# Kernel tuning notes

Measured on AMD Instinct MI355X. Metric: run time of the kernel, lower is better.

The kernel has to match this reference:

```python
import jax, jax.numpy as jnp
import numpy as np

B, T, HID = 1, 2048, 4096
H, KVH, D = 32, 8, 128
N_REP = H // KVH
SCALE = D ** -0.5
EPS = 1e-6
THETA = 10000.0
TOPK, SINK, WIN = 256, 16, 256


def _rms_norm(x, w):
    var = jnp.mean(x * x, axis=-1, keepdims=True)
    return w * (x * jax.lax.rsqrt(var + EPS))


def _rotate_half(x):
    x1, x2 = x[..., : D // 2], x[..., D // 2 :]
    return jnp.concatenate([-x2, x1], axis=-1)


def setup_inputs() -> dict:
    key = jax.random.key(0)
    ks = jax.random.split(key, 6)
    hidden_states = jax.random.normal(ks[0], (B, T, HID), jnp.float32)
    Wq = jax.random.normal(ks[1], (HID, H * D), jnp.float32) * 0.02
    Wkv = jax.random.normal(ks[2], (HID, KVH * D), jnp.float32) * 0.02
    Wo = jax.random.normal(ks[3], (H * D, HID), jnp.float32) * 0.02
    q_norm_w = jnp.ones((D,), jnp.float32)
    k_norm_w = jnp.ones((D,), jnp.float32)
    # standard RoPE tables, theta=10000
    inv_freq = 1.0 / (THETA ** (jnp.arange(0, D, 2, dtype=jnp.float32) / D))
    freqs = jnp.arange(T, dtype=jnp.float32)[:, None] * inv_freq[None, :]  # (T, D/2)
    emb = jnp.concatenate([freqs, freqs], axis=-1)  # (T, D)
    cos = jnp.cos(emb)[None]  # (1, T, D)
    sin = jnp.sin(emb)[None]
    return {"hidden_states": hidden_states, "Wq": Wq, "Wkv": Wkv, "Wo": Wo,
            "q_norm_w": q_norm_w, "k_norm_w": k_norm_w, "cos": cos, "sin": sin}


def reference(hidden_states, Wq, Wkv, Wo, q_norm_w, k_norm_w, cos, sin):
    b, t, _ = hidden_states.shape
    s = t
    # projections -> (b, h, t, d)
    q = (hidden_states @ Wq).reshape(b, t, H, D).transpose(0, 2, 1, 3)
    kv = (hidden_states @ Wkv).reshape(b, t, KVH, D).transpose(0, 2, 1, 3)
    # qk RMSNorm per head_dim
    q = _rms_norm(q, q_norm_w)
    k = _rms_norm(kv, k_norm_w)
    v = kv  # latent KV: value shares the latent projection (no norm / rope)
    # rotary, cos/sin unsqueezed at head dim
    c = cos[:, None]  # (1,1,T,D)
    sn = sin[:, None]
    q = q * c + _rotate_half(q) * sn
    k = k * c + _rotate_half(k) * sn
    # GQA expansion
    k = jnp.repeat(k, N_REP, axis=1)
    v = jnp.repeat(v, N_REP, axis=1)
    # dense scores (reference path)
    scores = jnp.einsum("bhtd,bhsd->bhts", q, k) * SCALE  # (b,h,t,s)
    # ---- sparse DSA mask: sink | local window | per-query top-k, then causal ----
    q_idx = jnp.arange(t)
    k_idx = jnp.arange(s)
    sink = (k_idx < SINK)[None, None, None, :]
    local = (jnp.abs(q_idx[:, None] - k_idx[None, :]) <= WIN)[None, None]
    kth = jax.lax.top_k(scores, TOPK)[0][..., -1:]  # k-th largest per query
    topk_keep = scores >= kth
    causal_ok = (k_idx[None, :] <= q_idx[:, None])[None, None]
    keep = (sink | local | topk_keep) & causal_ok
    scores = jnp.where(keep, scores, -jnp.inf)
    attn = jax.nn.softmax(scores, axis=-1)
    out = jnp.einsum("bhts,bhsd->bhtd", attn, v)
    out = out.transpose(0, 2, 1, 3).reshape(b, t, H * D)
    return out @ Wo
```

## Files before the change

kernel.cpp:

```cpp
#include <hip/hip_runtime.h>
#include <hip/hip_bf16.h>

#define H 32
#define KVH 8
#define D 128
#define T 2048
#define HID 4096
#define TOPK 256
#define SINK 16
#define WIN 256
#define SCALE 0.08838834764831845f
#define NPROJ 5120

#define SWZ(row, b) ((b) ^ (((row) & 7) << 4))

#define AS3(p) ((__attribute__((address_space(3))) void*)(p))
#define AS1(p) ((const __attribute__((address_space(1))) void*)(p))

typedef __attribute__((ext_vector_type(4))) float f32x4;
typedef __attribute__((ext_vector_type(8))) short short8;

__device__ __forceinline__ unsigned short f2bf(float f) {
  unsigned int b = __float_as_uint(f);
  b += 0x7FFFu + ((b >> 16) & 1u);
  return (unsigned short)(b >> 16);
}
__device__ __forceinline__ float bf2f(unsigned short u) {
  return __uint_as_float(((unsigned int)u) << 16);
}
__device__ __forceinline__ float ldf(const void* p, long i, bool b16) {
  return b16 ? bf2f(((const unsigned short*)p)[i]) : ((const float*)p)[i];
}
__device__ __forceinline__ bool bf16_mode(const unsigned int* probe) {
  return *probe == 0x3F803F80u;
}

__global__ void cvt_kernel(const void* __restrict__ src, unsigned short* __restrict__ dst,
                           long n, const unsigned int* probe) {
  bool b16 = bf16_mode(probe);
  long stride = (long)gridDim.x * blockDim.x;
  for (long i = (long)blockIdx.x * blockDim.x + threadIdx.x; i * 8 < n; i += stride) {
    long o = i * 8;
    if (b16) {
      *(uint4*)(dst + o) = *(const uint4*)((const unsigned short*)src + o);
    } else {
      const float* s = (const float*)src + o;
      float4 f0 = *(const float4*)s;
      float4 f1 = *(const float4*)(s + 4);
      uint4 v;
      v.x = (unsigned int)f2bf(f0.x) | ((unsigned int)f2bf(f0.y) << 16);
      v.y = (unsigned int)f2bf(f0.z) | ((unsigned int)f2bf(f0.w) << 16);
      v.z = (unsigned int)f2bf(f1.x) | ((unsigned int)f2bf(f1.y) << 16);
      v.w = (unsigned int)f2bf(f1.z) | ((unsigned int)f2bf(f1.w) << 16);
      *(uint4*)(dst + o) = v;
    }
  }
}

__global__ __launch_bounds__(256) void cvt_t(const void* __restrict__ src,
    unsigned short* __restrict__ dst, int R, int Cc, const unsigned int* probe) {
  __shared__ float tile[64][65];
  bool b16 = bf16_mode(probe);
  int r0 = blockIdx.y * 64, c0 = blockIdx.x * 64;
  int tid = threadIdx.x;
  int tr = tid >> 3;
  int tc8 = (tid & 7) * 8;
#pragma unroll
  for (int p = 0; p < 2; ++p) {
    int row = tr + p * 32;
    if (b16) {
      const unsigned short* s = (const unsigned short*)src + (size_t)(r0 + row) * Cc + c0 + tc8;
      uint4 d = *(const uint4*)s;
      const unsigned short* dv = (const unsigned short*)&d;
#pragma unroll
      for (int j = 0; j < 8; ++j) tile[row][tc8 + j] = bf2f(dv[j]);
    } else {
      const float* s = (const float*)src + (size_t)(r0 + row) * Cc + c0 + tc8;
      float4 f0 = *(const float4*)s;
      float4 f1 = *(const float4*)(s + 4);
      tile[row][tc8 + 0] = f0.x; tile[row][tc8 + 1] = f0.y;
      tile[row][tc8 + 2] = f0.z; tile[row][tc8 + 3] = f0.w;
      tile[row][tc8 + 4] = f1.x; tile[row][tc8 + 5] = f1.y;
      tile[row][tc8 + 6] = f1.z; tile[row][tc8 + 7] = f1.w;
    }
  }
  __syncthreads();
#pragma unroll
  for (int p = 0; p < 2; ++p) {
    int oc = tr + p * 32;
    unsigned short tmp[8];
#pragma unroll
    for (int j = 0; j < 8; ++j) tmp[j] = f2bf(tile[tc8 + j][oc]);
    *(uint4*)(dst + (size_t)(c0 + oc) * R + r0 + tc8) = *(uint4*)tmp;
  }
}

__global__ __launch_bounds__(256) void gemm_bf16(
    const unsigned short* __restrict__ A, const unsigned short* __restrict__ Bt,
    void* __restrict__ C, int M, int N, int K, const unsigned int* probe, int outmode) {
  __shared__ alignas(16) unsigned short As[128 * 32];
  __shared__ alignas(16) unsigned short Bs[128 * 32];
  int n0 = blockIdx.x * 128, m0 = blockIdx.y * 128;
  int tid = threadIdx.x;
  int w = tid >> 6, l = tid & 63;
  int wm = (w >> 1) * 64, wn = (w & 1) * 64;
  int lr = l & 15, lg = l >> 4;

  int srow0 = (w * 2 + 0) * 16 + (l >> 2);
  int srow1 = (w * 2 + 1) * 16 + (l >> 2);
  int cch = l & 3;
  int sf0 = (srow0 ^ (srow0 >> 2)) & 3;
  int sf1 = (srow1 ^ (srow1 >> 2)) & 3;
  const unsigned short* gA0 = A + (size_t)(m0 + srow0) * K + ((cch ^ sf0) * 8);
  const unsigned short* gA1 = A + (size_t)(m0 + srow1) * K + ((cch ^ sf1) * 8);
  const unsigned short* gB0 = Bt + (size_t)(n0 + srow0) * K + ((cch ^ sf0) * 8);
  const unsigned short* gB1 = Bt + (size_t)(n0 + srow1) * K + ((cch ^ sf1) * 8);
  unsigned short* lA0 = As + (w * 2 + 0) * 16 * 32;
  unsigned short* lA1 = As + (w * 2 + 1) * 16 * 32;
  unsigned short* lB0 = Bs + (w * 2 + 0) * 16 * 32;
  unsigned short* lB1 = Bs + (w * 2 + 1) * 16 * 32;

  const unsigned short* pa[4];
  const unsigned short* pb[4];
#pragma unroll
  for (int i = 0; i < 4; ++i) {
    int ra = wm + i * 16 + lr;
    int fa = (ra ^ (ra >> 2)) & 3;
    pa[i] = As + ra * 32 + ((lg ^ fa) * 8);
    int rb = wn + i * 16 + lr;
    int fb = (rb ^ (rb >> 2)) & 3;
    pb[i] = Bs + rb * 32 + ((lg ^ fb) * 8);
  }

  f32x4 zero = {0.f, 0.f, 0.f, 0.f};
  f32x4 acc[4][4];
#pragma unroll
  for (int i = 0; i < 4; ++i)
#pragma unroll
    for (int j = 0; j < 4; ++j) acc[i][j] = zero;

  for (int k0 = 0; k0 < K; k0 += 32) {
    __builtin_amdgcn_global_load_lds(AS1(gA0 + k0), AS3(lA0), 16, 0, 0);
    __builtin_amdgcn_global_load_lds(AS1(gA1 + k0), AS3(lA1), 16, 0, 0);
    __builtin_amdgcn_global_load_lds(AS1(gB0 + k0), AS3(lB0), 16, 0, 0);
    __builtin_amdgcn_global_load_lds(AS1(gB1 + k0), AS3(lB1), 16, 0, 0);
    __syncthreads();
    short8 a[4], b[4];
#pragma unroll
    for (int i = 0; i < 4; ++i) {
      a[i] = *(const short8*)pa[i];
      b[i] = *(const short8*)pb[i];
    }
#pragma unroll
    for (int i = 0; i < 4; ++i)
#pragma unroll
      for (int j = 0; j < 4; ++j)
        acc[i][j] = __builtin_amdgcn_mfma_f32_16x16x32_bf16(a[i], b[j], acc[i][j], 0, 0, 0);
    __syncthreads();
  }
  bool b16out = (outmode == 1) || (outmode == 2 && bf16_mode(probe));
#pragma unroll
  for (int i = 0; i < 4; ++i)
#pragma unroll
    for (int j = 0; j < 4; ++j)
#pragma unroll
      for (int r = 0; r < 4; ++r) {
        int row = m0 + wm + i * 16 + lg * 4 + r;
        int col = n0 + wn + j * 16 + lr;
        float v = acc[i][j][r];
        if (b16out) ((unsigned short*)C)[(size_t)row * N + col] = f2bf(v);
        else ((float*)C)[(size_t)row * N + col] = v;
      }
}

__global__ __launch_bounds__(256) void qk_prep(
    const unsigned short* __restrict__ Proj, const void* nw, const void* cosp, const void* sinp,
    unsigned short* __restrict__ Qh, const unsigned int* probe) {
  bool b16 = bf16_mode(probe);
  int w = threadIdx.x >> 6, l = threadIdx.x & 63;
  int gw = blockIdx.x * 4 + w;
  int t = gw >> 5, h = gw & 31;
  const unsigned short* x = Proj + (size_t)t * NPROJ + h * D;
  float x1 = bf2f(x[l]), x2 = bf2f(x[l + 64]);
  float s = x1 * x1 + x2 * x2;
  for (int m = 32; m; m >>= 1) s += __shfl_xor(s, m);
  float inv = rsqrtf(s * (1.0f / D) + 1e-6f);
  float w1 = ldf(nw, l, b16), w2 = ldf(nw, l + 64, b16);
  float c1 = ldf(cosp, (long)t * D + l, b16), c2 = ldf(cosp, (long)t * D + l + 64, b16);
  float s1 = ldf(sinp, (long)t * D + l, b16), s2 = ldf(sinp, (long)t * D + l + 64, b16);
  float xn1 = x1 * inv * w1, xn2 = x2 * inv * w2;
  unsigned short* o = Qh + (size_t)h * T * D + (size_t)t * D;
  o[l] = f2bf(SCALE * (xn1 * c1 - xn2 * s1));
  o[l + 64] = f2bf(SCALE * (xn2 * c2 + xn1 * s2));
}

__global__ __launch_bounds__(256) void kv_prep(
    const unsigned short* __restrict__ Proj, const void* nw, const void* cosp, const void* sinp,
    unsigned short* __restrict__ Kh, unsigned short* __restrict__ Vt, const unsigned int* probe) {
  bool b16 = bf16_mode(probe);
  int w = threadIdx.x >> 6, l = threadIdx.x & 63;
  int gw = blockIdx.x * 4 + w;
  int t = gw >> 3, h = gw & 7;
  const unsigned short* x = Proj + (size_t)t * NPROJ + (H * D) + h * D;
  float x1 = bf2f(x[l]), x2 = bf2f(x[l + 64]);
  Vt[(size_t)h * D * T + (size_t)l * T + t] = x[l];
  Vt[(size_t)h * D * T + (size_t)(l + 64) * T + t] = x[l + 64];
  float s = x1 * x1 + x2 * x2;
  for (int m = 32; m; m >>= 1) s += __shfl_xor(s, m);
  float inv = rsqrtf(s * (1.0f / D) + 1e-6f);
  float w1 = ldf(nw, l, b16), w2 = ldf(nw, l + 64, b16);
  float c1 = ldf(cosp, (long)t * D + l, b16), c2 = ldf(cosp, (long)t * D + l + 64, b16);
  float s1 = ldf(sinp, (long)t * D + l, b16), s2 = ldf(sinp, (long)t * D + l + 64, b16);
  float xn1 = x1 * inv * w1, xn2 = x2 * inv * w2;
  unsigned short* o = Kh + (size_t)h * T * D + (size_t)t * D;
  o[l] = f2bf(xn1 * c1 - xn2 * s1);
  o[l + 64] = f2bf(xn2 * c2 + xn1 * s2);
}

__global__ __launch_bounds__(1024, 8) void attn_kernel(
    const unsigned short* __restrict__ Qh, const unsigned short* __restrict__ Kh,
    const unsigned short* __restrict__ Vt, unsigned short* __restrict__ attn_out) {
  __shared__ alignas(16) unsigned short sc[16][2048];
  __shared__ alignas(16) unsigned short qt[16 * 128];
  __shared__ alignas(16) float part[8][64][4];
  __shared__ float zinv[16];
  int t0 = blockIdx.x * 16;
  int h = blockIdx.y;
  int hk = h >> 2;
  int tid = threadIdx.x;
  int w = tid >> 6, l = tid & 63;
  int lr = l & 15, lg = l >> 4;
  f32x4 zero = {0.f, 0.f, 0.f, 0.f};
  char* scB = (char*)sc;

  {
    int row = tid >> 6;
    int bir = (tid & 63) * 4;
    const unsigned int* qsrc = (const unsigned int*)(Qh + (size_t)h * (T * D) + (size_t)t0 * D);
    *(unsigned int*)((char*)qt + row * 256 + SWZ(row, bir)) = qsrc[tid];
  }
  __syncthreads();

  short8 aq[4];
#pragma unroll
  for (int kk = 0; kk < 4; ++kk)
    aq[kk] = *(const short8*)((const char*)qt + lr * 256 + SWZ(lr, kk * 64 + lg * 16));
  const unsigned short* Kbase = Kh + (size_t)hk * (T * D);
  for (int st = w; st < 128; st += 16) {
    f32x4 acc = zero;
#pragma unroll
    for (int kk = 0; kk < 4; ++kk) {
      short8 kf = *(const short8*)(Kbase + (size_t)(st * 16 + lr) * D + kk * 32 + lg * 8);
      acc = __builtin_amdgcn_mfma_f32_16x16x32_bf16(kf, aq[kk], acc, 0, 0, 0);
    }
    uint2 pk;
    pk.x = (unsigned int)f2bf(acc[0]) | ((unsigned int)f2bf(acc[1]) << 16);
    pk.y = (unsigned int)f2bf(acc[2]) | ((unsigned int)f2bf(acc[3]) << 16);
    *(uint2*)(scB + lr * 4096 + SWZ(lr, st * 32 + lg * 8)) = pk;
  }
  __syncthreads();

  {
    int row = w, tq = t0 + row;
    int rsw = (row & 7) << 4;
    char* rb = scB + row * 4096;
    unsigned int klo[16], khi[16];
#pragma unroll
    for (int i = 0; i < 16; ++i) {
      unsigned int b = *(const unsigned int*)(rb + ((256 * i + 4 * l) ^ rsw));
      unsigned int m = (b >> 15) & 0x00010001u;
      unsigned int kk = b ^ (0x80008000u | (m * 0x7FFFu));
      klo[i] = kk & 0xFFFFu;
      khi[i] = kk >> 16;
    }
    unsigned int lo = 0, hi = 0xFFFFu;
    while (lo < hi) {
      unsigned int mid = (lo + hi + 1u) >> 1;
      int c = 0;
#pragma unroll
      for (int i = 0; i < 16; ++i) {
        c += __popcll(__ballot(klo[i] >= mid));
        c += __popcll(__ballot(khi[i] >= mid));
      }
      if (c >= TOPK) lo = mid; else hi = mid - 1;
    }
    unsigned int thr = lo;
    unsigned int mA = 0, mB = 0, kmax = 0;
#pragma unroll
    for (int i = 0; i < 16; ++i) {
      int s0 = 128 * i + 2 * l;
      bool kp0 = (s0 <= tq) && (s0 < SINK || s0 + WIN >= tq || klo[i] >= thr);
      bool kp1 = (s0 + 1 <= tq) && (s0 + 1 < SINK || s0 + 1 + WIN >= tq || khi[i] >= thr);
      if (kp0) { mA |= (1u << i); kmax = kmax > klo[i] ? kmax : klo[i]; }
      if (kp1) { mB |= (1u << i); kmax = kmax > khi[i] ? kmax : khi[i]; }
    }
    for (int m = 32; m; m >>= 1) {
      unsigned int o = (unsigned int)__shfl_xor((int)kmax, m);
      kmax = kmax > o ? kmax : o;
    }
    unsigned int mb = (kmax & 0x8000u) ? (kmax ^ 0x8000u) : ((~kmax) & 0xFFFFu);
    float mx = bf2f((unsigned short)mb);
    float z = 0.f;
    int lim = (t0 + 15) >> 7;
#pragma unroll
    for (int i = 0; i < 16; ++i) if (i <= lim) {
      unsigned int k0 = klo[i], k1 = khi[i];
      unsigned int b0 = (k0 & 0x8000u) ? (k0 ^ 0x8000u) : ((~k0) & 0xFFFFu);
      unsigned int b1 = (k1 & 0x8000u) ? (k1 ^ 0x8000u) : ((~k1) & 0xFFFFu);
      float e0 = ((mA >> i) & 1u) ? __expf(bf2f((unsigned short)b0) - mx) : 0.f;
      float e1 = ((mB >> i) & 1u) ? __expf(bf2f((unsigned short)b1) - mx) : 0.f;
      z += e0 + e1;
      unsigned int pw = (unsigned int)f2bf(e0) | ((unsigned int)f2bf(e1) << 16);
      *(unsigned int*)(rb + ((256 * i + 4 * l) ^ rsw)) = pw;
    }
    for (int m = 32; m; m >>= 1) z += __shfl_xor(z, m);
    if (l == 0) zinv[row] = 1.0f / z;
  }
  __syncthreads();

  {
    int half = w >> 3;
    int d0 = (w & 7) * 16;
    const unsigned short* Vbase = Vt + (size_t)hk * (D * T);
    const char* prb = scB + lr * 4096;
    int psw = (lr & 7) << 4;
    f32x4 o0 = zero, o1 = zero;
    int ks_end = (t0 + 47) >> 5;
    int ks_endE = (ks_end + 1) & ~1;
    int kmid = ((ks_endE >> 1) + 1) & ~1;
    int ksA = half ? kmid : 0;
    int ksB = half ? ks_endE : kmid;
    for (int ks = ksA; ks < ksB; ks += 2) {
      short8 pa0 = *(const short8*)(prb + ((ks * 64 + lg * 16) ^ psw));
      short8 pa1 = *(const short8*)(prb + (((ks + 1) * 64 + lg * 16) ^ psw));
      short8 vb0 = *(const short8*)(Vbase + (size_t)(d0 + lr) * T + ks * 32 + lg * 8);
      short8 vb1 = *(const short8*)(Vbase + (size_t)(d0 + lr) * T + (ks + 1) * 32 + lg * 8);
      o0 = __builtin_amdgcn_mfma_f32_16x16x32_bf16(vb0, pa0, o0, 0, 0, 0);
      o1 = __builtin_amdgcn_mfma_f32_16x16x32_bf16(vb1, pa1, o1, 0, 0, 0);
    }
    f32x4 oo;
#pragma unroll
    for (int r = 0; r < 4; ++r) oo[r] = o0[r] + o1[r];
    if (half) *(f32x4*)(&part[w & 7][l][0]) = oo;
    __syncthreads();
    if (!half) {
      f32x4 po = *(const f32x4*)(&part[w & 7][l][0]);
      float rz = zinv[lr];
      unsigned short tmp[4];
#pragma unroll
      for (int r = 0; r < 4; ++r) tmp[r] = f2bf((oo[r] + po[r]) * rz);
      unsigned short* dst = attn_out + (size_t)(t0 + lr) * (H * D) + h * D + d0 + lg * 4;
      *(uint2*)dst = *(uint2*)tmp;
    }
  }
}

extern "C" void kernel_launch(void* const* d_in, const int* in_sizes, int n_in,
                              void* d_out, int out_size, void* d_ws, size_t ws_size,
                              hipStream_t stream) {
  (void)in_sizes; (void)n_in; (void)out_size; (void)ws_size;
  const void* hs = d_in[0];
  const void* Wq = d_in[1];
  const void* Wkv = d_in[2];
  const void* Wo = d_in[3];
  const unsigned int* probe = (const unsigned int*)d_in[4];
  const void* knw = d_in[5];
  const void* cosp = d_in[6];
  const void* sinp = d_in[7];

  char* ws = (char*)d_ws;
  unsigned short* WqT_bf = (unsigned short*)(ws);
  unsigned short* WkvT_bf= (unsigned short*)(ws + 33554432);
  unsigned short* WoT_bf = (unsigned short*)(ws + 41943040);
  unsigned short* hid_bf = (unsigned short*)(ws + 75497472);
  unsigned short* Proj_bf= (unsigned short*)(ws + 92274688);
  unsigned short* Qh     = (unsigned short*)(ws + 134217728);
  unsigned short* Kh     = (unsigned short*)(ws + 150994944);
  unsigned short* Vt     = (unsigned short*)(ws + 155189248);
  unsigned short* attn_bf= (unsigned short*)(ws + 159383552);

  hipLaunchKernelGGL(cvt_kernel, dim3(1024), dim3(256), 0, stream, hs, hid_bf, (long)T * HID, probe);
  hipLaunchKernelGGL(cvt_t, dim3(64, 64), dim3(256), 0, stream, Wq, WqT_bf, HID, H * D, probe);
  hipLaunchKernelGGL(cvt_t, dim3(16, 64), dim3(256), 0, stream, Wkv, WkvT_bf, HID, KVH * D, probe);
  hipLaunchKernelGGL(cvt_t, dim3(64, 64), dim3(256), 0, stream, Wo, WoT_bf, H * D, HID, probe);

  hipLaunchKernelGGL(gemm_bf16, dim3(40, 16), dim3(256), 0, stream,
                     hid_bf, WqT_bf, (void*)Proj_bf, 2048, NPROJ, 4096,
                     (const unsigned int*)nullptr, 1);

  hipLaunchKernelGGL(qk_prep, dim3(16384), dim3(256), 0, stream, Proj_bf, d_in[4], cosp, sinp, Qh, probe);
  hipLaunchKernelGGL(kv_prep, dim3(4096), dim3(256), 0, stream, Proj_bf, knw, cosp, sinp, Kh, Vt, probe);

  hipLaunchKernelGGL(attn_kernel, dim3(128, 32), dim3(1024), 0, stream, Qh, Kh, Vt, attn_bf);

  hipLaunchKernelGGL(gemm_bf16, dim3(32, 16), dim3(256), 0, stream,
                     attn_bf, WoT_bf, d_out, 2048, 4096, 4096, probe, 2);
}
```

Before: 764.3 us.

## Swizzle GEMM block order, narrow top-k bisection range, unroll attention loops

```diff
diff --git a/kernel.cpp b/kernel.cpp
--- a/kernel.cpp
+++ b/kernel.cpp
@@ -100,7 +100,11 @@
     void* __restrict__ C, int M, int N, int K, const unsigned int* probe, int outmode) {
   __shared__ alignas(16) unsigned short As[128 * 32];
   __shared__ alignas(16) unsigned short Bs[128 * 32];
-  int n0 = blockIdx.x * 128, m0 = blockIdx.y * 128;
+  int lin = blockIdx.x;
+  int qq = (int)gridDim.x >> 3;
+  int swz = (lin & 7) * qq + (lin >> 3);
+  int nx = N >> 7;
+  int n0 = (swz % nx) * 128, m0 = (swz / nx) * 128;
   int tid = threadIdx.x;
   int w = tid >> 6, l = tid & 63;
   int wm = (w >> 1) * 64, wn = (w & 1) * 64;
@@ -217,6 +221,9 @@
   o[l + 64] = f2bf(xn2 * c2 + xn1 * s2);
 }
 
+#define K16(X) X(0) X(1) X(2) X(3) X(4) X(5) X(6) X(7) \
+               X(8) X(9) X(10) X(11) X(12) X(13) X(14) X(15)
+
 __global__ __launch_bounds__(1024, 8) void attn_kernel(
     const unsigned short* __restrict__ Qh, const unsigned short* __restrict__ Kh,
     const unsigned short* __restrict__ Vt, unsigned short* __restrict__ attn_out) {
@@ -241,78 +248,104 @@
   }
   __syncthreads();
 
-  short8 aq[4];
-#pragma unroll
-  for (int kk = 0; kk < 4; ++kk)
-    aq[kk] = *(const short8*)((const char*)qt + lr * 256 + SWZ(lr, kk * 64 + lg * 16));
-  const unsigned short* Kbase = Kh + (size_t)hk * (T * D);
-  for (int st = w; st < 128; st += 16) {
-    f32x4 acc = zero;
-#pragma unroll
-    for (int kk = 0; kk < 4; ++kk) {
-      short8 kf = *(const short8*)(Kbase + (size_t)(st * 16 + lr) * D + kk * 32 + lg * 8);
-      acc = __builtin_amdgcn_mfma_f32_16x16x32_bf16(kf, aq[kk], acc, 0, 0, 0);
-    }
-    uint2 pk;
-    pk.x = (unsigned int)f2bf(acc[0]) | ((unsigned int)f2bf(acc[1]) << 16);
-    pk.y = (unsigned int)f2bf(acc[2]) | ((unsigned int)f2bf(acc[3]) << 16);
-    *(uint2*)(scB + lr * 4096 + SWZ(lr, st * 32 + lg * 8)) = pk;
+  {
+    short8 aq[4];
+#pragma unroll
+    for (int kk = 0; kk < 4; ++kk)
+      aq[kk] = *(const short8*)((const char*)qt + lr * 256 + SWZ(lr, kk * 64 + lg * 16));
+    const unsigned short* Kbase = Kh + (size_t)hk * (T * D);
+#pragma unroll 2
+    for (int st = w; st < 128; st += 16) {
+      f32x4 acc = zero;
+#pragma unroll
+      for (int kk = 0; kk < 4; ++kk) {
+        short8 kf = *(const short8*)(Kbase + (size_t)(st * 16 + lr) * D + kk * 32 + lg * 8);
+        acc = __builtin_amdgcn_mfma_f32_16x16x32_bf16(kf, aq[kk], acc, 0, 0, 0);
+      }
+      uint2 pk;
+      pk.x = (unsigned int)f2bf(acc[0]) | ((unsigned int)f2bf(acc[1]) << 16);
+      pk.y = (unsigned int)f2bf(acc[2]) | ((unsigned int)f2bf(acc[3]) << 16);
+      *(uint2*)(scB + lr * 4096 + SWZ(lr, st * 32 + lg * 8)) = pk;
+    }
   }
   __syncthreads();
 
   {
     int row = w, tq = t0 + row;
     int rsw = (row & 7) << 4;
+    int lim = (t0 + 15) >> 7;
     char* rb = scB + row * 4096;
-    unsigned int klo[16], khi[16];
-#pragma unroll
-    for (int i = 0; i < 16; ++i) {
-      unsigned int b = *(const unsigned int*)(rb + ((256 * i + 4 * l) ^ rsw));
-      unsigned int m = (b >> 15) & 0x00010001u;
-      unsigned int kk = b ^ (0x80008000u | (m * 0x7FFFu));
-      klo[i] = kk & 0xFFFFu;
-      khi[i] = kk >> 16;
-    }
-    unsigned int lo = 0, hi = 0xFFFFu;
+
+#define DECLK(i) unsigned int klo##i, khi##i;
+    K16(DECLK)
+#undef DECLK
+
+#define LOADK(i) { \
+      unsigned int b = *(const unsigned int*)(rb + ((256 * (i) + 4 * l) ^ rsw)); \
+      unsigned int m = (b >> 15) & 0x00010001u; \
+      b ^= (0x80008000u | (m * 0x7FFFu)); \
+      klo##i = b & 0xFFFFu; khi##i = b >> 16; }
+    K16(LOADK)
+#undef LOADK
+
+    unsigned int um = 0;
+#define MAXK(i) { um = um > klo##i ? um : klo##i; um = um > khi##i ? um : khi##i; }
+    K16(MAXK)
+#undef MAXK
+    for (int m = 32; m; m >>= 1) {
+      unsigned int o = (unsigned int)__shfl_xor((int)um, m);
+      um = um > o ? um : o;
+    }
+
+    unsigned int mid, lo, hi;
+    int cnt;
+#define CNT1(i) cnt += (int)__popcll(__ballot(klo##i >= mid)) + \
+                       (int)__popcll(__ballot(khi##i >= mid));
+    unsigned int probe = um > 2048u ? um - 2048u : 0u;
+    mid = probe; cnt = 0;
+    K16(CNT1)
+    if (cnt >= TOPK) { lo = probe; hi = um; }
+    else { lo = 0u; hi = probe - 1u; }
     while (lo < hi) {
-      unsigned int mid = (lo + hi + 1u) >> 1;
-      int c = 0;
-#pragma unroll
-      for (int i = 0; i < 16; ++i) {
-        c += __popcll(__ballot(klo[i] >= mid));
-        c += __popcll(__ballot(khi[i] >= mid));
-      }
-      if (c >= TOPK) lo = mid; else hi = mid - 1;
-    }
+      mid = (lo + hi + 1u) >> 1;
+      cnt = 0;
+      K16(CNT1)
+      if (cnt >= TOPK) lo = mid; else hi = mid - 1u;
+    }
+#undef CNT1
     unsigned int thr = lo;
-    unsigned int mA = 0, mB = 0, kmax = 0;
-#pragma unroll
-    for (int i = 0; i < 16; ++i) {
-      int s0 = 128 * i + 2 * l;
-      bool kp0 = (s0 <= tq) && (s0 < SINK || s0 + WIN >= tq || klo[i] >= thr);
-      bool kp1 = (s0 + 1 <= tq) && (s0 + 1 < SINK || s0 + 1 + WIN >= tq || khi[i] >= thr);
-      if (kp0) { mA |= (1u << i); kmax = kmax > klo[i] ? kmax : klo[i]; }
-      if (kp1) { mB |= (1u << i); kmax = kmax > khi[i] ? kmax : khi[i]; }
-    }
+
+    int ca0 = (tq - 2 * l) >> 7;
+    int ca1 = (tq - 2 * l - 1) >> 7;
+    int wa0 = (tq - WIN - 2 * l + 127) >> 7;
+    int wa1 = (tq - WIN - 2 * l - 1 + 127) >> 7;
+    bool snk = (l < 8);
+    unsigned int mA = 0, mB = 0, mk = 0;
+#define MASKK(i) if ((i) <= lim) { \
+      bool k0 = ((i) <= ca0) && ((((i) == 0) && snk) || ((i) >= wa0) || (klo##i >= thr)); \
+      bool k1 = ((i) <= ca1) && ((((i) == 0) && snk) || ((i) >= wa1) || (khi##i >= thr)); \
+      if (k0) { mA |= (1u << (i)); mk = mk > klo##i ? mk : klo##i; } \
+      if (k1) { mB |= (1u << (i)); mk = mk > khi##i ? mk : khi##i; } }
+    K16(MASKK)
+#undef MASKK
     for (int m = 32; m; m >>= 1) {
-      unsigned int o = (unsigned int)__shfl_xor((int)kmax, m);
-      kmax = kmax > o ? kmax : o;
-    }
-    unsigned int mb = (kmax & 0x8000u) ? (kmax ^ 0x8000u) : ((~kmax) & 0xFFFFu);
+      unsigned int o = (unsigned int)__shfl_xor((int)mk, m);
+      mk = mk > o ? mk : o;
+    }
+    unsigned int mb = (mk & 0x8000u) ? (mk ^ 0x8000u) : ((~mk) & 0xFFFFu);
     float mx = bf2f((unsigned short)mb);
+
     float z = 0.f;
-    int lim = (t0 + 15) >> 7;
-#pragma unroll
-    for (int i = 0; i < 16; ++i) if (i <= lim) {
-      unsigned int k0 = klo[i], k1 = khi[i];
-      unsigned int b0 = (k0 & 0x8000u) ? (k0 ^ 0x8000u) : ((~k0) & 0xFFFFu);
-      unsigned int b1 = (k1 & 0x8000u) ? (k1 ^ 0x8000u) : ((~k1) & 0xFFFFu);
-      float e0 = ((mA >> i) & 1u) ? __expf(bf2f((unsigned short)b0) - mx) : 0.f;
-      float e1 = ((mB >> i) & 1u) ? __expf(bf2f((unsigned short)b1) - mx) : 0.f;
-      z += e0 + e1;
-      unsigned int pw = (unsigned int)f2bf(e0) | ((unsigned int)f2bf(e1) << 16);
-      *(unsigned int*)(rb + ((256 * i + 4 * l) ^ rsw)) = pw;
-    }
+#define EXPK(i) if ((i) <= lim) { \
+      unsigned int b0 = (klo##i & 0x8000u) ? (klo##i ^ 0x8000u) : ((~klo##i) & 0xFFFFu); \
+      unsigned int b1 = (khi##i & 0x8000u) ? (khi##i ^ 0x8000u) : ((~khi##i) & 0xFFFFu); \
+      float e0 = ((mA >> (i)) & 1u) ? __expf(bf2f((unsigned short)b0) - mx) : 0.f; \
+      float e1 = ((mB >> (i)) & 1u) ? __expf(bf2f((unsigned short)b1) - mx) : 0.f; \
+      z += e0 + e1; \
+      *(unsigned int*)(rb + ((256 * (i) + 4 * l) ^ rsw)) = \
+          (unsigned int)f2bf(e0) | ((unsigned int)f2bf(e1) << 16); }
+    K16(EXPK)
+#undef EXPK
     for (int m = 32; m; m >>= 1) z += __shfl_xor(z, m);
     if (l == 0) zinv[row] = 1.0f / z;
   }
@@ -330,6 +363,7 @@
     int kmid = ((ks_endE >> 1) + 1) & ~1;
     int ksA = half ? kmid : 0;
     int ksB = half ? ks_endE : kmid;
+#pragma unroll 2
     for (int ks = ksA; ks < ksB; ks += 2) {
       short8 pa0 = *(const short8*)(prb + ((ks * 64 + lg * 16) ^ psw));
       short8 pa1 = *(const short8*)(prb + (((ks + 1) * 64 + lg * 16) ^ psw));
@@ -384,7 +418,7 @@
   hipLaunchKernelGGL(cvt_t, dim3(16, 64), dim3(256), 0, stream, Wkv, WkvT_bf, HID, KVH * D, probe);
   hipLaunchKernelGGL(cvt_t, dim3(64, 64), dim3(256), 0, stream, Wo, WoT_bf, H * D, HID, probe);
 
-  hipLaunchKernelGGL(gemm_bf16, dim3(40, 16), dim3(256), 0, stream,
+  hipLaunchKernelGGL(gemm_bf16, dim3(640), dim3(256), 0, stream,
                      hid_bf, WqT_bf, (void*)Proj_bf, 2048, NPROJ, 4096,
                      (const unsigned int*)nullptr, 1);
 
@@ -393,6 +427,6 @@
 
   hipLaunchKernelGGL(attn_kernel, dim3(128, 32), dim3(1024), 0, stream, Qh, Kh, Vt, attn_bf);
 
-  hipLaunchKernelGGL(gemm_bf16, dim3(32, 16), dim3(256), 0, stream,
+  hipLaunchKernelGGL(gemm_bf16, dim3(512), dim3(256), 0, stream,
                      attn_bf, WoT_bf, d_out, 2048, 4096, 4096, probe, 2);
 }
```

Measured after the change: 786.3 us. 2.9% more time.

## Swizzle GEMM blocks across XCDs, fold log2e into Q, and narrow the top-k search

Applied to the files above, without the earlier changes.

```diff
diff --git a/kernel.cpp b/kernel.cpp
--- a/kernel.cpp
+++ b/kernel.cpp
@@ -9,7 +9,7 @@
 #define TOPK 256
 #define SINK 16
 #define WIN 256
-#define SCALE 0.08838834764831845f
+#define SCALE2 0.12753102600893415f
 #define NPROJ 5120
 
 #define SWZ(row, b) ((b) ^ (((row) & 7) << 4))
@@ -100,7 +100,11 @@
     void* __restrict__ C, int M, int N, int K, const unsigned int* probe, int outmode) {
   __shared__ alignas(16) unsigned short As[128 * 32];
   __shared__ alignas(16) unsigned short Bs[128 * 32];
-  int n0 = blockIdx.x * 128, m0 = blockIdx.y * 128;
+  int lin = blockIdx.x;
+  int qq = (int)gridDim.x >> 3;
+  int swz = (lin & 7) * qq + (lin >> 3);
+  int nx = N >> 7;
+  int n0 = (swz % nx) * 128, m0 = (swz / nx) * 128;
   int tid = threadIdx.x;
   int w = tid >> 6, l = tid & 63;
   int wm = (w >> 1) * 64, wn = (w & 1) * 64;
@@ -190,8 +194,8 @@
   float s1 = ldf(sinp, (long)t * D + l, b16), s2 = ldf(sinp, (long)t * D + l + 64, b16);
   float xn1 = x1 * inv * w1, xn2 = x2 * inv * w2;
   unsigned short* o = Qh + (size_t)h * T * D + (size_t)t * D;
-  o[l] = f2bf(SCALE * (xn1 * c1 - xn2 * s1));
-  o[l + 64] = f2bf(SCALE * (xn2 * c2 + xn1 * s2));
+  o[l] = f2bf(SCALE2 * (xn1 * c1 - xn2 * s1));
+  o[l + 64] = f2bf(SCALE2 * (xn2 * c2 + xn1 * s2));
 }
 
 __global__ __launch_bounds__(256) void kv_prep(
@@ -241,77 +245,120 @@
   }
   __syncthreads();
 
-  short8 aq[4];
-#pragma unroll
-  for (int kk = 0; kk < 4; ++kk)
-    aq[kk] = *(const short8*)((const char*)qt + lr * 256 + SWZ(lr, kk * 64 + lg * 16));
-  const unsigned short* Kbase = Kh + (size_t)hk * (T * D);
-  for (int st = w; st < 128; st += 16) {
-    f32x4 acc = zero;
-#pragma unroll
-    for (int kk = 0; kk < 4; ++kk) {
-      short8 kf = *(const short8*)(Kbase + (size_t)(st * 16 + lr) * D + kk * 32 + lg * 8);
-      acc = __builtin_amdgcn_mfma_f32_16x16x32_bf16(kf, aq[kk], acc, 0, 0, 0);
-    }
-    uint2 pk;
-    pk.x = (unsigned int)f2bf(acc[0]) | ((unsigned int)f2bf(acc[1]) << 16);
-    pk.y = (unsigned int)f2bf(acc[2]) | ((unsigned int)f2bf(acc[3]) << 16);
-    *(uint2*)(scB + lr * 4096 + SWZ(lr, st * 32 + lg * 8)) = pk;
+  {
+    short8 aq[4];
+#pragma unroll
+    for (int kk = 0; kk < 4; ++kk)
+      aq[kk] = *(const short8*)((const char*)qt + lr * 256 + SWZ(lr, kk * 64 + lg * 16));
+    const unsigned short* Kbase = Kh + (size_t)hk * (T * D);
+#pragma unroll 2
+    for (int st = w; st < 128; st += 16) {
+      const unsigned short* kp = Kbase + (size_t)(st * 16 + lr) * D + lg * 8;
+      short8 kf0 = *(const short8*)(kp);
+      short8 kf1 = *(const short8*)(kp + 32);
+      short8 kf2 = *(const short8*)(kp + 64);
+      short8 kf3 = *(const short8*)(kp + 96);
+      f32x4 accA = zero, accB = zero;
+      accA = __builtin_amdgcn_mfma_f32_16x16x32_bf16(kf0, aq[0], accA, 0, 0, 0);
+      accB = __builtin_amdgcn_mfma_f32_16x16x32_bf16(kf1, aq[1], accB, 0, 0, 0);
+      accA = __builtin_amdgcn_mfma_f32_16x16x32_bf16(kf2, aq[2], accA, 0, 0, 0);
+      accB = __builtin_amdgcn_mfma_f32_16x16x32_bf16(kf3, aq[3], accB, 0, 0, 0);
+      uint2 pk;
+      pk.x = (unsigned int)f2bf(accA[0] + accB[0]) | ((unsigned int)f2bf(accA[1] + accB[1]) << 16);
+      pk.y = (unsigned int)f2bf(accA[2] + accB[2]) | ((unsigned int)f2bf(accA[3] + accB[3]) << 16);
+      *(uint2*)(scB + lr * 4096 + SWZ(lr, st * 32 + lg * 8)) = pk;
+    }
   }
   __syncthreads();
 
   {
     int row = w, tq = t0 + row;
     int rsw = (row & 7) << 4;
+    int lim = (t0 + 15) >> 7;
     char* rb = scB + row * 4096;
     unsigned int klo[16], khi[16];
 #pragma unroll
     for (int i = 0; i < 16; ++i) {
       unsigned int b = *(const unsigned int*)(rb + ((256 * i + 4 * l) ^ rsw));
       unsigned int m = (b >> 15) & 0x00010001u;
-      unsigned int kk = b ^ (0x80008000u | (m * 0x7FFFu));
-      klo[i] = kk & 0xFFFFu;
-      khi[i] = kk >> 16;
-    }
-    unsigned int lo = 0, hi = 0xFFFFu;
+      unsigned int kk2 = b ^ (0x80008000u | (m * 0x7FFFu));
+      klo[i] = kk2 & 0xFFFFu;
+      khi[i] = kk2 >> 16;
+    }
+    unsigned int um = 0;
+#pragma unroll
+    for (int i = 0; i < 16; ++i) {
+      unsigned int a_ = klo[i] > khi[i] ? klo[i] : khi[i];
+      um = um > a_ ? um : a_;
+    }
+    for (int m = 32; m; m >>= 1) {
+      unsigned int o = (unsigned int)__shfl_xor((int)um, m);
+      um = um > o ? um : o;
+    }
+    unsigned int lo = 0, hi = um;
+    {
+      unsigned int mid = um > 192u ? um - 192u : 1u;
+      int cnt = 0;
+#pragma unroll
+      for (int i = 0; i < 16; ++i)
+        cnt += (int)__popcll(__ballot(klo[i] >= mid)) + (int)__popcll(__ballot(khi[i] >= mid));
+      if (cnt >= TOPK) lo = mid; else hi = mid - 1u;
+    }
+    if (lo == 0u && um > 1024u) {
+      unsigned int mid = um - 1024u;
+      int cnt = 0;
+#pragma unroll
+      for (int i = 0; i < 16; ++i)
+        cnt += (int)__popcll(__ballot(klo[i] >= mid)) + (int)__popcll(__ballot(khi[i] >= mid));
+      if (cnt >= TOPK) lo = mid; else hi = mid - 1u;
+    }
     while (lo < hi) {
       unsigned int mid = (lo + hi + 1u) >> 1;
-      int c = 0;
-#pragma unroll
-      for (int i = 0; i < 16; ++i) {
-        c += __popcll(__ballot(klo[i] >= mid));
-        c += __popcll(__ballot(khi[i] >= mid));
-      }
-      if (c >= TOPK) lo = mid; else hi = mid - 1;
+      int cnt = 0;
+#pragma unroll
+      for (int i = 0; i < 16; ++i)
+        cnt += (int)__popcll(__ballot(klo[i] >= mid)) + (int)__popcll(__ballot(khi[i] >= mid));
+      if (cnt >= TOPK) lo = mid; else hi = mid - 1u;
     }
     unsigned int thr = lo;
-    unsigned int mA = 0, mB = 0, kmax = 0;
+
+    int ca0 = (tq - 2 * l) >> 7;
+    int ca1 = (tq - 2 * l - 1) >> 7;
+    int wa0 = (tq - WIN - 2 * l + 127) >> 7;
+    int wa1 = (tq - WIN - 2 * l - 1 + 127) >> 7;
+    bool snk = (l < 8);
+    unsigned int mA = 0, mB = 0, mk = 0;
 #pragma unroll
     for (int i = 0; i < 16; ++i) {
-      int s0 = 128 * i + 2 * l;
-      bool kp0 = (s0 <= tq) && (s0 < SINK || s0 + WIN >= tq || klo[i] >= thr);
-      bool kp1 = (s0 + 1 <= tq) && (s0 + 1 < SINK || s0 + 1 + WIN >= tq || khi[i] >= thr);
-      if (kp0) { mA |= (1u << i); kmax = kmax > klo[i] ? kmax : klo[i]; }
-      if (kp1) { mB |= (1u << i); kmax = kmax > khi[i] ? kmax : khi[i]; }
+      if (i > lim) break;
+      bool k0 = (i <= ca0) && (((i == 0) && snk) || (i >= wa0) || (klo[i] >= thr));
+      bool k1 = (i <= ca1) && (((i == 0) && snk) || (i >= wa1) || (khi[i] >= thr));
+      if (k0) { mA |= (1u << i); mk = mk > klo[i] ? mk : klo[i]; }
+      if (k1) { mB |= (1u << i); mk = mk > khi[i] ? mk : khi[i]; }
     }
     for (int m = 32; m; m >>= 1) {
-      unsigned int o = (unsigned int)__shfl_xor((int)kmax, m);
-      kmax = kmax > o ? kmax : o;
-    }
-    unsigned int mb = (kmax & 0x8000u) ? (kmax ^ 0x8000u) : ((~kmax) & 0xFFFFu);
+      unsigned int o = (unsigned int)__shfl_xor((int)mk, m);
+      mk = mk > o ? mk : o;
+    }
+    unsigned int mb = (mk & 0x8000u) ? (mk ^ 0x8000u) : ((~mk) & 0xFFFFu);
     float mx = bf2f((unsigned short)mb);
+
     float z = 0.f;
-    int lim = (t0 + 15) >> 7;
-#pragma unroll
-    for (int i = 0; i < 16; ++i) if (i <= lim) {
-      unsigned int k0 = klo[i], k1 = khi[i];
-      unsigned int b0 = (k0 & 0x8000u) ? (k0 ^ 0x8000u) : ((~k0) & 0xFFFFu);
-      unsigned int b1 = (k1 & 0x8000u) ? (k1 ^ 0x8000u) : ((~k1) & 0xFFFFu);
-      float e0 = ((mA >> i) & 1u) ? __expf(bf2f((unsigned short)b0) - mx) : 0.f;
-      float e1 = ((mB >> i) & 1u) ? __expf(bf2f((unsigned short)b1) - mx) : 0.f;
+#pragma unroll
+    for (int i = 0; i < 16; ++i) {
+      if (i > lim) break;
+      unsigned int b0 = (klo[i] & 0x8000u) ? (klo[i] ^ 0x8000u) : ((~klo[i]) & 0xFFFFu);
+      unsigned int b1 = (khi[i] & 0x8000u) ? (khi[i] ^ 0x8000u) : ((~khi[i]) & 0xFFFFu);
+      float x0 = bf2f((unsigned short)b0) - mx;
+      float x1 = bf2f((unsigned short)b1) - mx;
+      float e0x, e1x;
+      asm("v_exp_f32 %0, %1" : "=v"(e0x) : "v"(x0));
+      asm("v_exp_f32 %0, %1" : "=v"(e1x) : "v"(x1));
+      float e0 = ((mA >> i) & 1u) ? e0x : 0.f;
+      float e1 = ((mB >> i) & 1u) ? e1x : 0.f;
       z += e0 + e1;
-      unsigned int pw = (unsigned int)f2bf(e0) | ((unsigned int)f2bf(e1) << 16);
-      *(unsigned int*)(rb + ((256 * i + 4 * l) ^ rsw)) = pw;
+      *(unsigned int*)(rb + ((256 * i + 4 * l) ^ rsw)) =
+          (unsigned int)f2bf(e0) | ((unsigned int)f2bf(e1) << 16);
     }
     for (int m = 32; m; m >>= 1) z += __shfl_xor(z, m);
     if (l == 0) zinv[row] = 1.0f / z;
@@ -330,6 +377,7 @@
     int kmid = ((ks_endE >> 1) + 1) & ~1;
     int ksA = half ? kmid : 0;
     int ksB = half ? ks_endE : kmid;
+#pragma unroll 2
     for (int ks = ksA; ks < ksB; ks += 2) {
       short8 pa0 = *(const short8*)(prb + ((ks * 64 + lg * 16) ^ psw));
       short8 pa1 = *(const short8*)(prb + (((ks + 1) * 64 + lg * 16) ^ psw));
@@ -384,7 +432,7 @@
   hipLaunchKernelGGL(cvt_t, dim3(16, 64), dim3(256), 0, stream, Wkv, WkvT_bf, HID, KVH * D, probe);
   hipLaunchKernelGGL(cvt_t, dim3(64, 64), dim3(256), 0, stream, Wo, WoT_bf, H * D, HID, probe);
 
-  hipLaunchKernelGGL(gemm_bf16, dim3(40, 16), dim3(256), 0, stream,
+  hipLaunchKernelGGL(gemm_bf16, dim3(640), dim3(256), 0, stream,
                      hid_bf, WqT_bf, (void*)Proj_bf, 2048, NPROJ, 4096,
                      (const unsigned int*)nullptr, 1);
 
@@ -393,6 +441,6 @@
 
   hipLaunchKernelGGL(attn_kernel, dim3(128, 32), dim3(1024), 0, stream, Qh, Kh, Vt, attn_bf);
 
-  hipLaunchKernelGGL(gemm_bf16, dim3(32, 16), dim3(256), 0, stream,
+  hipLaunchKernelGGL(gemm_bf16, dim3(512), dim3(256), 0, stream,
                      attn_bf, WoT_bf, d_out, 2048, 4096, 4096, probe, 2);
 }
```

After: 750.5 us. About the same (-1.8%).
